# Kernel optimization log

Measured on AMD Instinct MI355X. Metric: run time of the kernel, lower is better.

Reference implementation:

```python
import jax, jax.numpy as jnp
import numpy as np

N_OBSERVED = 64
N_LATENT = 64
N_NODES = N_OBSERVED + N_LATENT
M = 2                # max parents per node (BA attachment param)
N_SAMPLES = 262144
CAL_N = 256
CAL_FRAC = 0.1
SIGMA_W = 1.0


def _build_dag():
    """BA-style DAG in topological order: node i picks min(M, i) earlier parents."""
    rng = np.random.default_rng(0)
    par_idx = np.zeros((N_NODES, M), np.int32)
    par_mask = np.zeros((N_NODES, M), np.float32)
    is_root = np.zeros(N_NODES, bool)
    for i in range(N_NODES):
        k = min(M, i)
        if k == 0:
            is_root[i] = True
            continue
        ps = rng.choice(i, size=k, replace=False)
        par_idx[i, :k] = ps
        par_mask[i, :k] = 1.0
    has_child = np.zeros(N_NODES, bool)
    for i in range(N_NODES):
        for j in range(M):
            if par_mask[i, j] > 0:
                has_child[par_idx[i, j]] = True
    leaves = np.where(~has_child)[0]
    pool = leaves if len(leaves) >= N_OBSERVED else np.arange(N_NODES)
    chosen = rng.choice(pool, size=N_OBSERVED, replace=False).astype(np.int32)
    return par_idx, par_mask, is_root, chosen


def setup_inputs() -> dict:
    par_idx, par_mask, is_root, chosen = _build_dag()
    wrng = np.random.default_rng(1)
    n_par = par_mask.sum(axis=1)
    std = SIGMA_W / np.sqrt(np.maximum(n_par, 1.0))  # nn.init.normal_(std=sigma_w/sqrt(n_parents))
    W = (wrng.standard_normal((N_NODES, M)) * std[:, None] * par_mask).astype(np.float32)
    b = np.zeros(N_NODES, np.float32)                # bias zero-initialised
    key = jax.random.key(0)
    k1, k2, k3 = jax.random.split(key, 3)
    return {
        "n_samples": N_SAMPLES,
        "W": jnp.asarray(W),
        "b": jnp.asarray(b),
        "root_pilot": jax.random.normal(k1, (N_NODES, CAL_N), jnp.float32),
        "root_main": jax.random.normal(k2, (N_NODES, N_SAMPLES), jnp.float32),
        "z_noise": jax.random.normal(k3, (N_NODES, N_SAMPLES), jnp.float32),
        "par_mask": jnp.asarray(par_mask),
        "par_idx": jnp.asarray(par_idx),
        "is_root": jnp.asarray(is_root),
        "chosen": jnp.asarray(chosen),
    }


def _run_dag(W, b, par_mask, par_idx, is_root, roots, noise):
    """Topological scan: x_i = relu(w_i . x_parents + b_i) + noise_i, roots ~ given."""
    n = roots.shape[1]

    def step(vals, inp):
        i, pidx, pmask, w, bb, root_v, nz, rt = inp
        pv = vals[pidx]                                   # [M, n] gather parents
        h = jax.nn.relu(jnp.einsum("p,pn->n", w * pmask, pv) + bb) + nz
        v = jnp.where(rt, root_v, h)
        v = jnp.where(jnp.isfinite(v), v, jnp.zeros_like(v))
        vals = jax.lax.dynamic_update_slice(vals, v[None, :], (i, 0))
        return vals, None

    vals0 = jnp.zeros((N_NODES, n), roots.dtype)
    xs = (jnp.arange(N_NODES), par_idx, par_mask, W, b, roots, noise, is_root)
    vals, _ = jax.lax.scan(step, vals0, xs)
    return vals


def reference(n_samples, W, b, root_pilot, root_main, z_noise, par_mask, par_idx, is_root, chosen):
    # noise calibration: noiseless pilot pass, sigma_e = frac * IQR per node
    pilot = _run_dag(W, b, par_mask, par_idx, is_root, root_pilot, jnp.zeros_like(root_pilot))
    q75 = jnp.quantile(pilot, 0.75, axis=1)
    q25 = jnp.quantile(pilot, 0.25, axis=1)
    sigma_e = CAL_FRAC * jnp.maximum(q75 - q25, 1e-6)     # [N_NODES]
    # main pass with calibrated per-node noise
    vals = _run_dag(W, b, par_mask, par_idx, is_root, root_main, z_noise * sigma_e[:, None])
    return vals[chosen].T                                  # [n_samples, n_observed]
```

## Files before the change

kernel.cpp:

```cpp
#include <hip/hip_runtime.h>
#include <hip/hip_bf16.h>
#include <math.h>

#define NN  128
#define BS  128
#define GRP 16

struct NodeP {
    float w0, w1, bb, sigma;
    int   p0, p1, root, pad;
};


__global__ __launch_bounds__(128) void prep_kernel(
    const float* __restrict__ W, const float* __restrict__ b,
    const float* __restrict__ pm, const int* __restrict__ pidx,
    const float* __restrict__ root_main, const float* __restrict__ z,
    size_t NS, NodeP* __restrict__ params, const float** __restrict__ srcs)
{
    int i = threadIdx.x;
    if (i < NN) {
        float m0 = pm[2 * i], m1 = pm[2 * i + 1];
        NodeP p;
        p.w0 = W[2 * i] * m0;
        p.w1 = W[2 * i + 1] * m1;
        p.bb = b[i];
        p.sigma = 0.0f;
        p.p0 = pidx[2 * i];
        p.p1 = pidx[2 * i + 1];
        p.root = (m0 + m1 == 0.0f) ? 1 : 0;
        p.pad = 0;
        params[i] = p;
        srcs[i] = (p.root ? root_main : z) + (size_t)i * NS;
    }
}

__global__ __launch_bounds__(128) void pilot_kernel(
    const NodeP* __restrict__ params, const float* __restrict__ root_pilot,
    float* __restrict__ pilot_out, int CAL)
{
    __shared__ float vals[NN * BS];
    const int tid = threadIdx.x;
    const int j = blockIdx.x * BS + tid;
    for (int i = 0; i < NN; ++i) {
        NodeP p = params[i];
        float v;
        if (p.root) {
            v = root_pilot[(size_t)i * CAL + j];
        } else {
            float a = vals[p.p0 * BS + (tid ^ (p.p0 & 31))];
            float c = vals[p.p1 * BS + (tid ^ (p.p1 & 31))];
            v = fmaxf(fmaf(p.w0, a, fmaf(p.w1, c, p.bb)), 0.0f);
        }
        if (!isfinite(v)) v = 0.0f;
        vals[i * BS + (tid ^ (i & 31))] = v;
        pilot_out[(size_t)i * CAL + j] = v;
    }
}

__global__ __launch_bounds__(256) void quant_kernel(
    const float* __restrict__ pilot, NodeP* __restrict__ params, int CAL)
{
    __shared__ float s[256];
    const int tid = threadIdx.x;
    const int node = blockIdx.x;
    s[tid] = pilot[(size_t)node * CAL + tid];
    __syncthreads();
    for (int k = 2; k <= 256; k <<= 1) {
        for (int jj = k >> 1; jj > 0; jj >>= 1) {
            int ixj = tid ^ jj;
            if (ixj > tid) {
                float a = s[tid], bv = s[ixj];
                bool up = ((tid & k) == 0);
                if ((a > bv) == up) { s[tid] = bv; s[ixj] = a; }
            }
            __syncthreads();
        }
    }
    if (tid == 0) {
        float q25 = s[63]  + 0.75f * (s[64]  - s[63]);
        float q75 = s[191] + 0.25f * (s[192] - s[191]);
        params[node].sigma = 0.1f * fmaxf(q75 - q25, 1e-6f);
    }
}

__global__ __launch_bounds__(128) void main_kernel(
    const NodeP* __restrict__ params, const float* const* __restrict__ srcs,
    const int* __restrict__ chosen, float* __restrict__ out, size_t NS)
{
    __shared__ float vals[NN * BS];
    const int tid = threadIdx.x;
    const size_t j = (size_t)blockIdx.x * BS + tid;

    float zb[2][GRP];
    #pragma unroll
    for (int u = 0; u < GRP; ++u) zb[0][u] = srcs[u][j];

    #pragma unroll
    for (int g = 0; g < NN / GRP; ++g) {
        if (g + 1 < NN / GRP) {
            #pragma unroll
            for (int u = 0; u < GRP; ++u)
                zb[(g + 1) & 1][u] = srcs[(g + 1) * GRP + u][j];
        }
        #pragma unroll
        for (int u = 0; u < GRP; ++u) {
            int i = g * GRP + u;
            NodeP p = params[i];
            float zv = zb[g & 1][u];
            float v;
            if (p.root) {
                v = zv;
            } else {
                float a = vals[p.p0 * BS + (tid ^ (p.p0 & 31))];
                float c = vals[p.p1 * BS + (tid ^ (p.p1 & 31))];
                v = fmaxf(fmaf(p.w0, a, fmaf(p.w1, c, p.bb)), 0.0f) + p.sigma * zv;
            }
            if (!isfinite(v)) v = 0.0f;
            vals[i * BS + (tid ^ (i & 31))] = v;
        }
    }

    __syncthreads();

    float4* out4 = (float4*)(out + (size_t)blockIdx.x * BS * 64);
    #pragma unroll
    for (int it = 0; it < 16; ++it) {
        int c  = it * BS + tid;
        int s  = c >> 4;
        int k0 = (c & 15) << 2;
        int n0 = chosen[k0 + 0], n1 = chosen[k0 + 1];
        int n2 = chosen[k0 + 2], n3 = chosen[k0 + 3];
        float4 o;
        o.x = vals[n0 * BS + (s ^ (n0 & 31))];
        o.y = vals[n1 * BS + (s ^ (n1 & 31))];
        o.z = vals[n2 * BS + (s ^ (n2 & 31))];
        o.w = vals[n3 * BS + (s ^ (n3 & 31))];
        out4[c] = o;
    }
}

extern "C" void kernel_launch(void* const* d_in, const int* in_sizes, int n_in,
                              void* d_out, int out_size, void* d_ws, size_t ws_size,
                              hipStream_t stream) {
    const float* W          = (const float*)d_in[1];
    const float* b          = (const float*)d_in[2];
    const float* root_pilot = (const float*)d_in[3];
    const float* root_main  = (const float*)d_in[4];
    const float* z          = (const float*)d_in[5];
    const float* pm         = (const float*)d_in[6];
    const int*   pidx       = (const int*)d_in[7];
    const int*   chosen     = (const int*)d_in[9];
    float* out = (float*)d_out;

    const size_t NS  = (size_t)in_sizes[4] / NN;
    const int    CAL = in_sizes[3] / NN;

    char* ws = (char*)d_ws;
    NodeP*        params = (NodeP*)ws;
    const float** srcs   = (const float**)(ws + 4096);
    float*        pilot  = (float*)(ws + 8192);

    prep_kernel<<<1, 128, 0, stream>>>(W, b, pm, pidx, root_main, z, NS, params, srcs);
    pilot_kernel<<<CAL / BS, BS, 0, stream>>>(params, root_pilot, pilot, CAL);
    quant_kernel<<<NN, 256, 0, stream>>>(pilot, params, CAL);
    main_kernel<<<(int)(NS / BS), BS, 0, stream>>>(params, srcs, chosen, out, NS);
}
```

Measured before the change: 367.8 us.

## Schedule DAG nodes by depth level and deepen noise-load prefetch pipeline

The prep kernel computes each node's depth in the DAG and emits a level-ordered schedule padded to groups of 8 (padding repeats a node so the duplicate writes are idempotent). Main and pilot kernels walk that schedule so nodes within a group have no intra-group dependencies, and main prefetches noise and root values several groups ahead in registers. Block size drops from 128 to 64 threads, halving shared memory per block to allow more resident blocks. It adds indirection through index tables and higher register pressure from the deeper prefetch buffers.

```diff
diff --git a/kernel.cpp b/kernel.cpp
--- a/kernel.cpp
+++ b/kernel.cpp
@@ -2,64 +2,98 @@
 #include <hip/hip_bf16.h>
 #include <math.h>
 
-#define NN  128
-#define BS  128
-#define GRP 16
-
-struct NodeP {
-    float w0, w1, bb, sigma;
-    int   p0, p1, root, pad;
-};
+#define NN    128
+#define BS    64
+#define G     8
+#define CH    4
+#define SCAP  2048
+#define SCAPS 1024
+#define ROOTF (1 << 30)
 
 
 __global__ __launch_bounds__(128) void prep_kernel(
     const float* __restrict__ W, const float* __restrict__ b,
     const float* __restrict__ pm, const int* __restrict__ pidx,
-    const float* __restrict__ root_main, const float* __restrict__ z,
-    size_t NS, NodeP* __restrict__ params, const float** __restrict__ srcs)
-{
-    int i = threadIdx.x;
-    if (i < NN) {
-        float m0 = pm[2 * i], m1 = pm[2 * i + 1];
-        NodeP p;
-        p.w0 = W[2 * i] * m0;
-        p.w1 = W[2 * i + 1] * m1;
-        p.bb = b[i];
-        p.sigma = 0.0f;
-        p.p0 = pidx[2 * i];
-        p.p1 = pidx[2 * i + 1];
-        p.root = (m0 + m1 == 0.0f) ? 1 : 0;
-        p.pad = 0;
-        params[i] = p;
-        srcs[i] = (p.root ? root_main : z) + (size_t)i * NS;
-    }
-}
-
-__global__ __launch_bounds__(128) void pilot_kernel(
-    const NodeP* __restrict__ params, const float* __restrict__ root_pilot,
-    float* __restrict__ pilot_out, int CAL)
+    float4* __restrict__ wf, int* __restrict__ pk,
+    int* __restrict__ zidx, int* __restrict__ ngp)
+{
+    __shared__ int dep[NN], cnt[NN], lst[NN + 1], sidx[SCAPS];
+    __shared__ int mx, total;
+    const int i = threadIdx.x;
+    float m0 = pm[2 * i], m1 = pm[2 * i + 1];
+    int   p0 = pidx[2 * i], p1 = pidx[2 * i + 1];
+    int   rt = (m0 == 0.0f && m1 == 0.0f) ? 1 : 0;
+    wf[i] = make_float4(W[2 * i] * m0, W[2 * i + 1] * m1, b[i], 0.0f);
+    pk[i] = p0 | (p1 << 8) | (rt << 16);
+
+    dep[i] = 0; cnt[i] = 0;
+    if (i == 0) { mx = 0; }
+    __syncthreads();
+    for (int it = 0; it < NN; ++it) {
+        int nd = rt ? 0 : 1 + max(dep[p0], dep[p1]);
+        int ch = (nd != dep[i]);
+        dep[i] = nd;
+        if (__syncthreads_count(ch) == 0) break;
+    }
+    int l = dep[i];
+    atomicMax(&mx, l);
+    int r = atomicAdd(&cnt[l], 1);
+    __syncthreads();
+    if (i == 0) {
+        int acc = 0;
+        for (int q = 0; q <= mx; ++q) { lst[q] = acc; acc += (cnt[q] + G - 1) & ~(G - 1); }
+        lst[mx + 1] = acc;
+        total = acc;
+        ngp[0] = acc / G;
+    }
+    __syncthreads();
+    int code = i | (rt ? ROOTF : 0);
+    sidx[lst[l] + r] = code;
+    if (r == 0) {
+        int lend = lst[l] + ((cnt[l] + G - 1) & ~(G - 1));
+        for (int q = lst[l] + cnt[l]; q < lend; ++q) sidx[q] = code;
+    }
+    __syncthreads();
+    int tl = total;
+    for (int k = i; k < SCAP; k += NN) zidx[k] = sidx[k < tl ? k : tl - 1];
+}
+
+__global__ __launch_bounds__(64) void pilot_kernel(
+    const float4* __restrict__ wf, const int* __restrict__ pk,
+    const int* __restrict__ zidx, const int* __restrict__ ngp,
+    const float* __restrict__ root_pilot, float* __restrict__ pilot_out, int CAL)
 {
     __shared__ float vals[NN * BS];
     const int tid = threadIdx.x;
-    const int j = blockIdx.x * BS + tid;
-    for (int i = 0; i < NN; ++i) {
-        NodeP p = params[i];
-        float v;
-        if (p.root) {
-            v = root_pilot[(size_t)i * CAL + j];
-        } else {
-            float a = vals[p.p0 * BS + (tid ^ (p.p0 & 31))];
-            float c = vals[p.p1 * BS + (tid ^ (p.p1 & 31))];
-            v = fmaxf(fmaf(p.w0, a, fmaf(p.w1, c, p.bb)), 0.0f);
-        }
-        if (!isfinite(v)) v = 0.0f;
-        vals[i * BS + (tid ^ (i & 31))] = v;
-        pilot_out[(size_t)i * CAL + j] = v;
+    const int jj  = blockIdx.x * BS + tid;
+    const int ng  = ngp[0];
+    for (int g = 0; g < ng; ++g) {
+        int cd[G], pkv[G]; float4 w[G];
+        #pragma unroll
+        for (int u = 0; u < G; ++u) cd[u] = zidx[g * G + u];
+        #pragma unroll
+        for (int u = 0; u < G; ++u) { int n = cd[u] & 0xffff; pkv[u] = pk[n]; w[u] = wf[n]; }
+        #pragma unroll
+        for (int u = 0; u < G; ++u) {
+            int n = cd[u] & 0xffff;
+            float v;
+            if (pkv[u] & 0x10000) {
+                v = root_pilot[(size_t)n * CAL + jj];
+            } else {
+                int q0 = pkv[u] & 0xff, q1 = (pkv[u] >> 8) & 0xff;
+                float a = vals[q0 * BS + (tid ^ (q0 & 31))];
+                float c = vals[q1 * BS + (tid ^ (q1 & 31))];
+                v = fmaxf(fmaf(w[u].x, a, fmaf(w[u].y, c, w[u].z)), 0.0f);
+            }
+            if (!isfinite(v)) v = 0.0f;
+            vals[n * BS + (tid ^ (n & 31))] = v;
+            pilot_out[(size_t)n * CAL + jj] = v;
+        }
     }
 }
 
 __global__ __launch_bounds__(256) void quant_kernel(
-    const float* __restrict__ pilot, NodeP* __restrict__ params, int CAL)
+    const float* __restrict__ pilot, float4* __restrict__ wf, int CAL)
 {
     __shared__ float s[256];
     const int tid = threadIdx.x;
@@ -80,57 +114,112 @@
     if (tid == 0) {
         float q25 = s[63]  + 0.75f * (s[64]  - s[63]);
         float q75 = s[191] + 0.25f * (s[192] - s[191]);
-        params[node].sigma = 0.1f * fmaxf(q75 - q25, 1e-6f);
-    }
-}
-
-__global__ __launch_bounds__(128) void main_kernel(
-    const NodeP* __restrict__ params, const float* const* __restrict__ srcs,
+        ((float*)&wf[node])[3] = 0.1f * fmaxf(q75 - q25, 1e-6f);
+    }
+}
+
+__device__ __forceinline__ void do_chunk(
+    int gg, int (&ccur)[CH][G], int (&cnxt)[CH][G],
+    int (&pkb)[2][G], float4 (&wfb)[2][G], float (&zbuf)[CH][G],
+    const int* __restrict__ zidx, const int* __restrict__ pk,
+    const float4* __restrict__ wf,
+    const float* __restrict__ root_main, const float* __restrict__ z,
+    size_t NS, size_t j, float* vals, int tid)
+{
+    #pragma unroll
+    for (int s = 0; s < CH; ++s)
+        #pragma unroll
+        for (int u = 0; u < G; ++u)
+            cnxt[s][u] = zidx[(gg + 1) * CH * G + s * G + u];
+
+    #pragma unroll
+    for (int s = 0; s < CH; ++s) {
+        #pragma unroll
+        for (int u = 0; u < G; ++u) {
+            int cN = (s < CH - 1) ? ccur[s + 1][u] : cnxt[0][u];
+            int n  = cN & 0xffff;
+            pkb[(s + 1) & 1][u] = pk[n];
+            wfb[(s + 1) & 1][u] = wf[n];
+        }
+        float zv[G];
+        #pragma unroll
+        for (int u = 0; u < G; ++u) zv[u] = zbuf[s][u];
+        #pragma unroll
+        for (int u = 0; u < G; ++u) {
+            int c = cnxt[s][u];
+            const float* base = (c & ROOTF) ? root_main : z;
+            zbuf[s][u] = base[(size_t)(c & 0xffff) * NS + j];
+        }
+        #pragma unroll
+        for (int u = 0; u < G; ++u) {
+            int   pkv = pkb[s & 1][u];
+            float4 w  = wfb[s & 1][u];
+            float v;
+            if (pkv & 0x10000) {
+                v = zv[u];
+            } else {
+                int q0 = pkv & 0xff, q1 = (pkv >> 8) & 0xff;
+                float a = vals[q0 * BS + (tid ^ (q0 & 31))];
+                float c2 = vals[q1 * BS + (tid ^ (q1 & 31))];
+                v = fmaxf(fmaf(w.x, a, fmaf(w.y, c2, w.z)), 0.0f) + w.w * zv[u];
+            }
+            if (!isfinite(v)) v = 0.0f;
+            int n = ccur[s][u] & 0xffff;
+            vals[n * BS + (tid ^ (n & 31))] = v;
+        }
+    }
+}
+
+__global__ __launch_bounds__(64) void main_kernel(
+    const float4* __restrict__ wf, const int* __restrict__ pk,
+    const int* __restrict__ zidx, const int* __restrict__ ngp,
+    const float* __restrict__ root_main, const float* __restrict__ z,
     const int* __restrict__ chosen, float* __restrict__ out, size_t NS)
 {
     __shared__ float vals[NN * BS];
     const int tid = threadIdx.x;
     const size_t j = (size_t)blockIdx.x * BS + tid;
-
-    float zb[2][GRP];
-    #pragma unroll
-    for (int u = 0; u < GRP; ++u) zb[0][u] = srcs[u][j];
-
-    #pragma unroll
-    for (int g = 0; g < NN / GRP; ++g) {
-        if (g + 1 < NN / GRP) {
-            #pragma unroll
-            for (int u = 0; u < GRP; ++u)
-                zb[(g + 1) & 1][u] = srcs[(g + 1) * GRP + u][j];
-        }
-        #pragma unroll
-        for (int u = 0; u < GRP; ++u) {
-            int i = g * GRP + u;
-            NodeP p = params[i];
-            float zv = zb[g & 1][u];
-            float v;
-            if (p.root) {
-                v = zv;
-            } else {
-                float a = vals[p.p0 * BS + (tid ^ (p.p0 & 31))];
-                float c = vals[p.p1 * BS + (tid ^ (p.p1 & 31))];
-                v = fmaxf(fmaf(p.w0, a, fmaf(p.w1, c, p.bb)), 0.0f) + p.sigma * zv;
-            }
-            if (!isfinite(v)) v = 0.0f;
-            vals[i * BS + (tid ^ (i & 31))] = v;
-        }
-    }
-
-    __syncthreads();
-
+    const int ng  = ngp[0];
+    const int ngc = (ng + CH - 1) / CH;
+
+    int    codesA[CH][G], codesB[CH][G];
+    int    pkb[2][G];
+    float4 wfb[2][G];
+    float  zbuf[CH][G];
+
+    #pragma unroll
+    for (int s = 0; s < CH; ++s)
+        #pragma unroll
+        for (int u = 0; u < G; ++u)
+            codesA[s][u] = zidx[s * G + u];
+    #pragma unroll
+    for (int s = 0; s < CH; ++s)
+        #pragma unroll
+        for (int u = 0; u < G; ++u) {
+            int c = codesA[s][u];
+            const float* base = (c & ROOTF) ? root_main : z;
+            zbuf[s][u] = base[(size_t)(c & 0xffff) * NS + j];
+        }
+    #pragma unroll
+    for (int u = 0; u < G; ++u) {
+        int n = codesA[0][u] & 0xffff;
+        pkb[0][u] = pk[n];
+        wfb[0][u] = wf[n];
+    }
+
+    for (int gg = 0; gg < ngc; gg += 2) {
+        do_chunk(gg,     codesA, codesB, pkb, wfb, zbuf, zidx, pk, wf, root_main, z, NS, j, vals, tid);
+        do_chunk(gg + 1, codesB, codesA, pkb, wfb, zbuf, zidx, pk, wf, root_main, z, NS, j, vals, tid);
+    }
+
+    __syncthreads();
     float4* out4 = (float4*)(out + (size_t)blockIdx.x * BS * 64);
     #pragma unroll
     for (int it = 0; it < 16; ++it) {
         int c  = it * BS + tid;
         int s  = c >> 4;
         int k0 = (c & 15) << 2;
-        int n0 = chosen[k0 + 0], n1 = chosen[k0 + 1];
-        int n2 = chosen[k0 + 2], n3 = chosen[k0 + 3];
+        int n0 = chosen[k0], n1 = chosen[k0 + 1], n2 = chosen[k0 + 2], n3 = chosen[k0 + 3];
         float4 o;
         o.x = vals[n0 * BS + (s ^ (n0 & 31))];
         o.y = vals[n1 * BS + (s ^ (n1 & 31))];
@@ -157,12 +246,14 @@
     const int    CAL = in_sizes[3] / NN;
 
     char* ws = (char*)d_ws;
-    NodeP*        params = (NodeP*)ws;
-    const float** srcs   = (const float**)(ws + 4096);
-    float*        pilot  = (float*)(ws + 8192);
-
-    prep_kernel<<<1, 128, 0, stream>>>(W, b, pm, pidx, root_main, z, NS, params, srcs);
-    pilot_kernel<<<CAL / BS, BS, 0, stream>>>(params, root_pilot, pilot, CAL);
-    quant_kernel<<<NN, 256, 0, stream>>>(pilot, params, CAL);
-    main_kernel<<<(int)(NS / BS), BS, 0, stream>>>(params, srcs, chosen, out, NS);
-}
+    float4* wf    = (float4*)ws;
+    int*    pk    = (int*)(ws + 2048);
+    int*    zidx  = (int*)(ws + 4096);
+    int*    ngp   = (int*)(ws + 12288);
+    float*  pilot = (float*)(ws + 16384);
+
+    prep_kernel <<<1, 128, 0, stream>>>(W, b, pm, pidx, wf, pk, zidx, ngp);
+    pilot_kernel<<<CAL / BS, BS, 0, stream>>>(wf, pk, zidx, ngp, root_pilot, pilot, CAL);
+    quant_kernel<<<NN, 256, 0, stream>>>(pilot, wf, CAL);
+    main_kernel <<<(int)(NS / BS), BS, 0, stream>>>(wf, pk, zidx, ngp, root_main, z, chosen, out, NS);
+}
```

Measured after the change: 468.5 us. +27.4%, slower.
